# Performance work log

Hardware: AMD Instinct MI355X
Metric: run time of the kernel (lower is better)

Reference implementation:

```python
import jax, jax.numpy as jnp
import numpy as np

NUM_SEGMENTS = 128  # batch_size * alpha_iter


def setup_inputs() -> dict:
    key = jax.random.key(0)
    ks = jax.random.split(key, 16)
    T, E, H, C, O = 131072, 256, 512, 256, 32
    words = jax.random.normal(ks[0], (T, E), dtype=jnp.float32)
    seg_ids = jnp.sort(jax.random.randint(ks[1], (T,), 0, NUM_SEGMENTS))
    def lin(kw, kb, fi, fo):
        s = 1.0 / np.sqrt(fi)
        return (jax.random.uniform(kw, (fi, fo), minval=-s, maxval=s, dtype=jnp.float32),
                jax.random.uniform(kb, (fo,), minval=-s, maxval=s, dtype=jnp.float32))
    W1, b1 = lin(ks[2], ks[3], E, H)
    W2, b2 = lin(ks[4], ks[5], H, H)
    W3, b3 = lin(ks[6], ks[7], H, C)
    P1, pb1 = lin(ks[8], ks[9], C, H)
    P2, pb2 = lin(ks[10], ks[11], H, H)
    P3, pb3 = lin(ks[12], ks[13], H, O)
    return {"words": words, "seg_ids": seg_ids,
            "W1": W1, "b1": b1, "W2": W2, "b2": b2, "W3": W3, "b3": b3,
            "P1": P1, "pb1": pb1, "P2": P2, "pb2": pb2, "P3": P3, "pb3": pb3,
            "batch_size": 16, "alpha_iter": 8}


def reference(words, seg_ids, W1, b1, W2, b2, W3, b3,
              P1, pb1, P2, pb2, P3, pb3, batch_size, alpha_iter):
    # encoder MLP on every token: Linear-tanh-Linear-tanh-Linear
    h = jnp.tanh(words @ W1 + b1)
    h = jnp.tanh(h @ W2 + b2)
    tok_enc = h @ W3 + b3                                  # [T, enc_dim]
    # per-set sum pooling (ragged sum over each word tensor)
    enc = jax.ops.segment_sum(tok_enc, seg_ids, num_segments=batch_size * alpha_iter)
    # predictor MLP
    p = jnp.tanh(enc @ P1 + pb1)
    p = jnp.tanh(p @ P2 + pb2)
    pred = p @ P3 + pb3                                    # [B*A, target_dim]
    return pred.reshape(batch_size, alpha_iter, -1)
```

## Files before the change

kernel.cpp:

```cpp
#include <hip/hip_runtime.h>
#include <hip/hip_bf16.h>
#include <hip/hip_fp16.h>


typedef _Float16 half8v __attribute__((ext_vector_type(8)));
typedef _Float16 half4v __attribute__((ext_vector_type(4)));
typedef __fp16 fp16x2 __attribute__((ext_vector_type(2)));
typedef float f32x4 __attribute__((ext_vector_type(4)));
typedef float f32x16 __attribute__((ext_vector_type(16)));

#define TANH_SCALE 2.8853900817779268f
#define E_STRF 65

__device__ __forceinline__ unsigned pkrtz(float a, float b) {
    fp16x2 p = __builtin_amdgcn_cvt_pkrtz(a, b);
    return __builtin_bit_cast(unsigned, p);
}

__global__ __launch_bounds__(256) void wt_kernel(
    const float* __restrict__ W1, const float* __restrict__ W2,
    const float* __restrict__ W3,
    _Float16* __restrict__ F1, _Float16* __restrict__ F2,
    _Float16* __restrict__ F3) {
    int u = blockIdx.x * 256 + threadIdx.x;
    const float* W; _Float16* F; int FW, NFT, u0; float scale;
    if (u < 16384)      { W = W1; F = F1; FW = 512; NFT = 16; u0 = u;         scale = TANH_SCALE; }
    else if (u < 49152) { W = W2; F = F2; FW = 512; NFT = 16; u0 = u - 16384; scale = TANH_SCALE; }
    else                { W = W3; F = F3; FW = 256; NFT = 8;  u0 = u - 49152; scale = 1.0f; }
    int lane = u0 & 63, frag = u0 >> 6;
    int ft = frag % NFT, ks = frag / NFT;
    int f = ft * 32 + (lane & 31);
    int k0 = ks * 16 + (lane >> 5) * 8;
    half8v v;
    #pragma unroll
    for (int j = 0; j < 8; ++j)
        v[j] = (_Float16)(W[(size_t)(k0 + j) * FW + f] * scale);
    *(half8v*)((char*)F + (size_t)u0 * 16) = v;
}

template<int K, int MT, int NFT>
__device__ __forceinline__ void mlp_pass32(const char* __restrict__ F, int wave,
                                           const char* lds_act,
                                           const float* sbias_layer, int lane,
                                           f32x16 acc[MT][2]) {
    const int r2 = lane & 31;
    const int hi = lane >> 5;
    const int fbase = wave * (MT * 32);
    #pragma unroll
    for (int mt = 0; mt < MT; ++mt)
        #pragma unroll
        for (int q = 0; q < 4; ++q) {
            f32x4 bv = *(const f32x4*)(sbias_layer + fbase + mt * 32 + hi * 4 + q * 8);
            #pragma unroll
            for (int j = 0; j < 4; ++j) {
                acc[mt][0][q * 4 + j] = bv[j];
                acc[mt][1][q * 4 + j] = bv[j];
            }
        }
    const char* fb = F + ((size_t)wave * MT) * 1024 + lane * 16;
    const int xm = (r2 & 15) << 4;
    const char* bb = lds_act + (size_t)r2 * 1024;

    constexpr int NS = K / 16;
    half8v A[3][MT], B[2][2];
    #pragma unroll
    for (int mt = 0; mt < MT; ++mt) {
        A[0][mt] = *(const half8v*)(fb + mt * 1024);
        A[1][mt] = *(const half8v*)(fb + (NFT + mt) * 1024);
    }
    #pragma unroll
    for (int nt = 0; nt < 2; ++nt)
        B[0][nt] = *(const half8v*)(bb + nt * 32768 + ((hi * 16) ^ xm));

    #pragma unroll
    for (int s = 0; s < NS; ++s) {
        if (s + 2 < NS) {
            #pragma unroll
            for (int mt = 0; mt < MT; ++mt)
                A[(s + 2) % 3][mt] =
                    *(const half8v*)(fb + ((size_t)(s + 2) * NFT + mt) * 1024);
        }
        if (s + 1 < NS) {
            int off = ((((s + 1) * 32) | (hi * 16)) ^ xm);
            #pragma unroll
            for (int nt = 0; nt < 2; ++nt)
                B[(s + 1) & 1][nt] = *(const half8v*)(bb + nt * 32768 + off);
        }
        __builtin_amdgcn_s_setprio(1);
        #pragma unroll
        for (int nt = 0; nt < 2; ++nt)
            #pragma unroll
            for (int mt = 0; mt < MT; ++mt)
                acc[mt][nt] = __builtin_amdgcn_mfma_f32_32x32x16_f16(
                    A[s % 3][mt], B[s & 1][nt], acc[mt][nt], 0, 0, 0);
        __builtin_amdgcn_s_setprio(0);
    }
}

template<int MT>
__device__ __forceinline__ void store_h32(char* lds_out, const f32x16 acc[MT][2],
                                          int fbase, int lane) {
    const int t_lo = lane & 31;
    const int hi = lane >> 5;
    #pragma unroll
    for (int mt = 0; mt < MT; ++mt)
        #pragma unroll
        for (int nt = 0; nt < 2; ++nt) {
            int t = nt * 32 + t_lo;
            int xm = (t & 15) << 4;
            #pragma unroll
            for (int q = 0; q < 4; ++q) {
                int chunk = (fbase >> 3) + mt * 4 + q;
                float th[4];
                #pragma unroll
                for (int j = 0; j < 4; ++j) {
                    float e = __builtin_amdgcn_exp2f(acc[mt][nt][q * 4 + j]);
                    float rr = __builtin_amdgcn_rcpf(e + 1.0f);
                    th[j] = fmaf(-2.0f, rr, 1.0f);
                }
                uint2 u = { pkrtz(th[0], th[1]), pkrtz(th[2], th[3]) };
                *(uint2*)(lds_out + t * 1024 + ((chunk << 4) ^ xm) + hi * 8) = u;
            }
        }
}

__global__ __launch_bounds__(512, 4) void encoder_kernel(
    const float* __restrict__ words, const int* __restrict__ seg_ids,
    const _Float16* __restrict__ F1, const _Float16* __restrict__ F2,
    const _Float16* __restrict__ F3,
    const float* __restrict__ b1, const float* __restrict__ b2,
    const float* __restrict__ b3, float* __restrict__ enc) {
    __shared__ __align__(16) char buf[66560];
    __shared__ __align__(16) float sbias[1280];
    __shared__ int sseg[64];

    const int tid = threadIdx.x;
    const int lane = tid & 63;
    const int wave = tid >> 6;
    const int tok0 = blockIdx.x * 64;

    sbias[tid] = b1[tid] * TANH_SCALE;
    sbias[512 + tid] = b2[tid] * TANH_SCALE;
    if (tid < 256) sbias[1024 + tid] = b3[tid];
    if (tid < 64) sseg[tid] = seg_ids[tok0 + tid];

    const float* wsrc = words + (size_t)tok0 * 256;
    #pragma unroll
    for (int it = 0; it < 8; ++it) {
        int i = it * 512 + tid;
        float4 v = ((const float4*)wsrc)[i];
        int t = i >> 6;
        int col = i & 63;
        uint2 u = { pkrtz(v.x, v.y), pkrtz(v.z, v.w) };
        int off = t * 1024 + (((col >> 1) << 4) ^ ((t & 15) << 4)) + (col & 1) * 8;
        *(uint2*)(buf + off) = u;
    }
    __syncthreads();

    {
        f32x16 acc[2][2];
        mlp_pass32<256, 2, 16>((const char*)F1, wave, buf, sbias, lane, acc);
        __syncthreads();
        store_h32<2>(buf, acc, wave * 64, lane);
    }
    __syncthreads();

    {
        f32x16 acc[2][2];
        mlp_pass32<512, 2, 16>((const char*)F2, wave, buf, sbias + 512, lane, acc);
        __syncthreads();
        store_h32<2>(buf, acc, wave * 64, lane);
    }
    __syncthreads();

    {
        f32x16 acc[1][2];
        mlp_pass32<512, 1, 8>((const char*)F3, wave, buf, sbias + 1024, lane, acc);
        __syncthreads();
        float* encT = (float*)buf;
        const int t_lo = lane & 31;
        const int hi = lane >> 5;
        #pragma unroll
        for (int nt = 0; nt < 2; ++nt) {
            int t = nt * 32 + t_lo;
            #pragma unroll
            for (int q = 0; q < 4; ++q) {
                int f0 = wave * 32 + hi * 4 + q * 8;
                #pragma unroll
                for (int j = 0; j < 4; ++j)
                    encT[(f0 + j) * E_STRF + t] = acc[0][nt][q * 4 + j];
            }
        }
    }
    __syncthreads();

    {
        int f = tid & 255;
        int hh = tid >> 8;
        int t0 = hh * 32;
        const float* encT = (const float*)buf;
        float a = 0.0f;
        int cur = sseg[t0];
        for (int i = 0; i < 32; ++i) {
            int t = t0 + i;
            float v = encT[f * E_STRF + t];
            int s = sseg[t];
            if (s != cur) { atomicAdd(&enc[cur * 256 + f], a); a = 0.0f; cur = s; }
            a += v;
        }
        atomicAdd(&enc[cur * 256 + f], a);
    }
}

__global__ __launch_bounds__(256) void pred_kernel(
    const float* __restrict__ enc,
    const float* __restrict__ P1, const float* __restrict__ pb1,
    const float* __restrict__ P2, const float* __restrict__ pb2,
    const float* __restrict__ P3, const float* __restrict__ pb3,
    float* __restrict__ out) {
    __shared__ float se[256];
    __shared__ float sp[512];
    __shared__ float red[256];
    const int tid = threadIdx.x, b = blockIdx.x;
    se[tid] = enc[b * 256 + tid];
    __syncthreads();
    float a0 = pb1[tid], a1 = pb1[tid + 256];
    for (int k = 0; k < 256; ++k) {
        float e = se[k];
        a0 = fmaf(e, P1[k * 512 + tid], a0);
        a1 = fmaf(e, P1[k * 512 + tid + 256], a1);
    }
    sp[tid] = tanhf(a0);
    sp[tid + 256] = tanhf(a1);
    __syncthreads();
    a0 = pb2[tid]; a1 = pb2[tid + 256];
    for (int k = 0; k < 512; ++k) {
        float p = sp[k];
        a0 = fmaf(p, P2[k * 512 + tid], a0);
        a1 = fmaf(p, P2[k * 512 + tid + 256], a1);
    }
    __syncthreads();
    sp[tid] = tanhf(a0);
    sp[tid + 256] = tanhf(a1);
    __syncthreads();
    int j = tid & 31, part = tid >> 5;
    float s = 0.0f;
    for (int k = part * 64; k < part * 64 + 64; ++k)
        s = fmaf(sp[k], P3[k * 32 + j], s);
    red[tid] = s;
    __syncthreads();
    if (tid < 128) red[tid] += red[tid + 128];
    __syncthreads();
    if (tid < 64) red[tid] += red[tid + 64];
    __syncthreads();
    if (tid < 32) out[b * 32 + tid] = red[tid] + red[tid + 32] + pb3[tid];
}

extern "C" void kernel_launch(void* const* d_in, const int* in_sizes, int n_in,
                              void* d_out, int out_size, void* d_ws, size_t ws_size,
                              hipStream_t stream) {
    const float* words = (const float*)d_in[0];
    const int* seg_ids = (const int*)d_in[1];
    const float* W1 = (const float*)d_in[2];
    const float* b1 = (const float*)d_in[3];
    const float* W2 = (const float*)d_in[4];
    const float* b2 = (const float*)d_in[5];
    const float* W3 = (const float*)d_in[6];
    const float* b3 = (const float*)d_in[7];
    const float* P1 = (const float*)d_in[8];
    const float* pb1 = (const float*)d_in[9];
    const float* P2 = (const float*)d_in[10];
    const float* pb2 = (const float*)d_in[11];
    const float* P3 = (const float*)d_in[12];
    const float* pb3 = (const float*)d_in[13];
    float* out = (float*)d_out;

    char* ws = (char*)d_ws;
    _Float16* F1 = (_Float16*)(ws);
    _Float16* F2 = (_Float16*)(ws + 262144);
    _Float16* F3 = (_Float16*)(ws + 786432);
    float* enc = (float*)(ws + 1048576);

    (void)hipMemsetAsync(enc, 0, 128 * 256 * 4, stream);
    wt_kernel<<<256, 256, 0, stream>>>(W1, W2, W3, F1, F2, F3);
    encoder_kernel<<<2048, 512, 0, stream>>>(words, seg_ids, F1, F2, F3,
                                             b1, b2, b3, enc);
    pred_kernel<<<128, 256, 0, stream>>>(enc, P1, pb1, P2, pb2, P3, pb3, out);
}
```

Baseline: 212.4 us.

## Double encoder token tile to 128 with 16 waves split over features and tokens

The encoder block now processes 128 tokens with 1024 threads. Waves are arranged as 8 feature groups by 2 token halves, so each pair of waves shares the same weight fragments within a block. Blocks fall from 2048 to 1024, which halves the total weight-fragment traffic streamed per token. The cost is more LDS per block (about 137 KB, likely one block per CU), larger block-wide barriers with 16 waves, and no overlap between co-resident blocks. The pooling transpose stride is widened to fit the extra tokens.

```diff
diff --git a/kernel.cpp b/kernel.cpp
--- a/kernel.cpp
+++ b/kernel.cpp
@@ -10,7 +10,7 @@
 typedef float f32x16 __attribute__((ext_vector_type(16)));
 
 #define TANH_SCALE 2.8853900817779268f
-#define E_STRF 65
+#define E_STRF 129
 
 __device__ __forceinline__ unsigned pkrtz(float a, float b) {
     fp16x2 p = __builtin_amdgcn_cvt_pkrtz(a, b);
@@ -39,13 +39,13 @@
 }
 
 template<int K, int MT, int NFT>
-__device__ __forceinline__ void mlp_pass32(const char* __restrict__ F, int wave,
-                                           const char* lds_act,
+__device__ __forceinline__ void mlp_pass32(const char* __restrict__ F, int fw,
+                                           int tokofs, const char* lds_act,
                                            const float* sbias_layer, int lane,
                                            f32x16 acc[MT][2]) {
     const int r2 = lane & 31;
     const int hi = lane >> 5;
-    const int fbase = wave * (MT * 32);
+    const int fbase = fw * (MT * 32);
     #pragma unroll
     for (int mt = 0; mt < MT; ++mt)
         #pragma unroll
@@ -57,9 +57,9 @@
                 acc[mt][1][q * 4 + j] = bv[j];
             }
         }
-    const char* fb = F + ((size_t)wave * MT) * 1024 + lane * 16;
+    const char* fb = F + ((size_t)fw * MT) * 1024 + lane * 16;
     const int xm = (r2 & 15) << 4;
-    const char* bb = lds_act + (size_t)r2 * 1024;
+    const char* bb = lds_act + (size_t)(tokofs + r2) * 1024;
 
     constexpr int NS = K / 16;
     half8v A[3][MT], B[2][2];
@@ -99,14 +99,14 @@
 
 template<int MT>
 __device__ __forceinline__ void store_h32(char* lds_out, const f32x16 acc[MT][2],
-                                          int fbase, int lane) {
+                                          int fbase, int tokofs, int lane) {
     const int t_lo = lane & 31;
     const int hi = lane >> 5;
     #pragma unroll
     for (int mt = 0; mt < MT; ++mt)
         #pragma unroll
         for (int nt = 0; nt < 2; ++nt) {
-            int t = nt * 32 + t_lo;
+            int t = tokofs + nt * 32 + t_lo;
             int xm = (t & 15) << 4;
             #pragma unroll
             for (int q = 0; q < 4; ++q) {
@@ -124,30 +124,31 @@
         }
 }
 
-__global__ __launch_bounds__(512, 4) void encoder_kernel(
+__global__ __launch_bounds__(1024, 4) void encoder_kernel(
     const float* __restrict__ words, const int* __restrict__ seg_ids,
     const _Float16* __restrict__ F1, const _Float16* __restrict__ F2,
     const _Float16* __restrict__ F3,
     const float* __restrict__ b1, const float* __restrict__ b2,
     const float* __restrict__ b3, float* __restrict__ enc) {
-    __shared__ __align__(16) char buf[66560];
+    __shared__ __align__(16) char buf[132096];
     __shared__ __align__(16) float sbias[1280];
-    __shared__ int sseg[64];
+    __shared__ int sseg[128];
 
     const int tid = threadIdx.x;
     const int lane = tid & 63;
     const int wave = tid >> 6;
-    const int tok0 = blockIdx.x * 64;
-
-    sbias[tid] = b1[tid] * TANH_SCALE;
-    sbias[512 + tid] = b2[tid] * TANH_SCALE;
+    const int fw = wave >> 1, tw = wave & 1;
+    const int tok0 = blockIdx.x * 128;
+
+    if (tid < 512) sbias[tid] = b1[tid] * TANH_SCALE;
+    else           sbias[tid] = b2[tid - 512] * TANH_SCALE;
     if (tid < 256) sbias[1024 + tid] = b3[tid];
-    if (tid < 64) sseg[tid] = seg_ids[tok0 + tid];
+    if (tid < 128) sseg[tid] = seg_ids[tok0 + tid];
 
     const float* wsrc = words + (size_t)tok0 * 256;
     #pragma unroll
     for (int it = 0; it < 8; ++it) {
-        int i = it * 512 + tid;
+        int i = it * 1024 + tid;
         float4 v = ((const float4*)wsrc)[i];
         int t = i >> 6;
         int col = i & 63;
@@ -159,33 +160,33 @@
 
     {
         f32x16 acc[2][2];
-        mlp_pass32<256, 2, 16>((const char*)F1, wave, buf, sbias, lane, acc);
+        mlp_pass32<256, 2, 16>((const char*)F1, fw, tw * 64, buf, sbias, lane, acc);
         __syncthreads();
-        store_h32<2>(buf, acc, wave * 64, lane);
+        store_h32<2>(buf, acc, fw * 64, tw * 64, lane);
     }
     __syncthreads();
 
     {
         f32x16 acc[2][2];
-        mlp_pass32<512, 2, 16>((const char*)F2, wave, buf, sbias + 512, lane, acc);
+        mlp_pass32<512, 2, 16>((const char*)F2, fw, tw * 64, buf, sbias + 512, lane, acc);
         __syncthreads();
-        store_h32<2>(buf, acc, wave * 64, lane);
+        store_h32<2>(buf, acc, fw * 64, tw * 64, lane);
     }
     __syncthreads();
 
     {
         f32x16 acc[1][2];
-        mlp_pass32<512, 1, 8>((const char*)F3, wave, buf, sbias + 1024, lane, acc);
+        mlp_pass32<512, 1, 8>((const char*)F3, fw, tw * 64, buf, sbias + 1024, lane, acc);
         __syncthreads();
         float* encT = (float*)buf;
         const int t_lo = lane & 31;
         const int hi = lane >> 5;
         #pragma unroll
         for (int nt = 0; nt < 2; ++nt) {
-            int t = nt * 32 + t_lo;
+            int t = tw * 64 + nt * 32 + t_lo;
             #pragma unroll
             for (int q = 0; q < 4; ++q) {
-                int f0 = wave * 32 + hi * 4 + q * 8;
+                int f0 = fw * 32 + hi * 4 + q * 8;
                 #pragma unroll
                 for (int j = 0; j < 4; ++j)
                     encT[(f0 + j) * E_STRF + t] = acc[0][nt][q * 4 + j];
@@ -196,8 +197,8 @@
 
     {
         int f = tid & 255;
-        int hh = tid >> 8;
-        int t0 = hh * 32;
+        int qq = tid >> 8;
+        int t0 = qq * 32;
         const float* encT = (const float*)buf;
         float a = 0.0f;
         int cur = sseg[t0];
@@ -283,7 +284,7 @@
 
     (void)hipMemsetAsync(enc, 0, 128 * 256 * 4, stream);
     wt_kernel<<<256, 256, 0, stream>>>(W1, W2, W3, F1, F2, F3);
-    encoder_kernel<<<2048, 512, 0, stream>>>(words, seg_ids, F1, F2, F3,
-                                             b1, b2, b3, enc);
+    encoder_kernel<<<1024, 1024, 0, stream>>>(words, seg_ids, F1, F2, F3,
+                                              b1, b2, b3, enc);
     pred_kernel<<<128, 256, 0, stream>>>(enc, P1, pb1, P2, pb2, P3, pb3, out);
 }
```

Result: slower. 225.2 us (+6.0%).
